# Kernel tuning notes

Measured on AMD Instinct MI355X. Metric: run time of the kernel, lower is better.

## Reference

```python
import jax, jax.numpy as jnp
import numpy as np


def setup_inputs() -> dict:
    key = jax.random.key(0)
    kq, kk, kv = jax.random.split(key, 3)
    N, T, F = 16, 2048, 128
    q = jax.random.normal(kq, (N, T, F), dtype=jnp.float32)
    k = jax.random.normal(kk, (N, T, F), dtype=jnp.float32)
    v = jax.random.normal(kv, (N, T, F), dtype=jnp.float32)
    return {"q": q, "k": k, "v": v, "masked": 1}


def reference(q, k, v, masked):
    # scores: [N, T, T] = q @ k^T / sqrt(F)
    F = q.shape[-1]
    scores = jnp.einsum("ntf,nsf->nts", q, k) / jnp.sqrt(jnp.asarray(F, q.dtype))
    if masked:
        T = q.shape[1]
        causal = jnp.tril(jnp.ones((T, T), dtype=bool))  # [T, T]
        scores = jnp.where(causal[None, :, :], scores, jnp.asarray(-1e9, scores.dtype))
    attn = jax.nn.softmax(scores, axis=-1)
    # dropout is identity in eval/reference mode
    return jnp.einsum("nts,nsf->ntf", attn, v)
```

## Files before the change

kernel.cpp:

```cpp
#include <hip/hip_runtime.h>
#include <hip/hip_bf16.h>
#include <stdint.h>

#define T_SEQ 2048
#define DH    128
#define BKV   64
#define QSCALE 0.12751742796f
#define SLOT_F 8320
#define WS_NEEDED 55115776ULL

typedef short  short8 __attribute__((ext_vector_type(8)));
typedef __bf16 bf16x8 __attribute__((ext_vector_type(8)));
typedef float  f32x4  __attribute__((ext_vector_type(4)));

__device__ __forceinline__ bf16x8 as_bf16x8(short8 x) { return __builtin_bit_cast(bf16x8, x); }

__device__ __forceinline__ uint32_t bf_bits(float x) {
  union { __hip_bfloat16 h; unsigned short u; } cv;
  cv.h = __float2bfloat16(x);
  return (uint32_t)cv.u;
}

__global__ void convert_bf16(const float* __restrict__ src, unsigned short* __restrict__ dst,
                             int n4) {
  int i = blockIdx.x * 256 + threadIdx.x;
  if (i >= n4) return;
  const float4 f = ((const float4*)src)[i];
  union { unsigned short us[4]; uint2 u2; } o;
  o.us[0] = (unsigned short)bf_bits(f.x);
  o.us[1] = (unsigned short)bf_bits(f.y);
  o.us[2] = (unsigned short)bf_bits(f.z);
  o.us[3] = (unsigned short)bf_bits(f.w);
  ((uint2*)dst)[i] = o.u2;
}

__global__ void transpose_v_bf16(const float* __restrict__ v, unsigned short* __restrict__ vt) {
  __shared__ float tile[64][65];
  const int n = blockIdx.z, d0 = blockIdx.y * 64, t0 = blockIdx.x * 64;
  const int tx = threadIdx.x, ty = threadIdx.y;
  #pragma unroll
  for (int i = 0; i < 64; i += 8)
    tile[ty + i][tx] = v[((size_t)n * T_SEQ + t0 + ty + i) * DH + d0 + tx];
  __syncthreads();
  #pragma unroll
  for (int i = 0; i < 64; i += 8)
    vt[((size_t)n * DH + d0 + ty + i) * T_SEQ + t0 + tx] = (unsigned short)bf_bits(tile[tx][ty + i]);
}

__global__ __launch_bounds__(256, 4) void attn_fwd(
    const float* __restrict__ Qf,
    const unsigned short* __restrict__ Kb,
    const unsigned short* __restrict__ Vt,
    float* __restrict__ Out,
    float* __restrict__ Part,
    const int* __restrict__ maskp,
    int use_split)
{
  __shared__ __align__(16) char smem[32768];

  const int tid  = threadIdx.x;
  const int lane = tid & 63;
  const int w    = tid >> 6;
  const int m15  = lane & 15;
  const int g    = lane >> 4;

  const int bid = blockIdx.x;
  const int n   = (bid & 7) + 8 * ((bid >> 3) & 1);
  const int job = bid >> 4;
  const int masked = maskp[0];

  int qt, c, k0, k1, nc;
  if (masked && use_split) {
    int base = 0; qt = 0;
    for (;;) { int ncq = (qt + 8) >> 3; if (job < base + ncq) { c = job - base; break; } base += ncq; ++qt; }
    nc = (qt + 8) >> 3;
    k0 = c * 8;
    k1 = min(k0 + 8, qt + 1);
  } else {
    if (job >= 32) return;
    qt = job; c = 0; nc = 1; k0 = 0;
    k1 = masked ? (qt + 1) : (T_SEQ / BKV);
  }

  const int qrow = qt * 64 + 16 * w + m15;

  bf16x8 qf[4];
  {
    const float* qg = Qf + ((size_t)n * T_SEQ + qrow) * DH;
    #pragma unroll
    for (int kf = 0; kf < 4; ++kf) {
      const float4 f0 = *(const float4*)(qg + 32 * kf + 8 * g);
      const float4 f1 = *(const float4*)(qg + 32 * kf + 8 * g + 4);
      union { unsigned short us[8]; short8 s8; } qa;
      qa.us[0] = (unsigned short)bf_bits(f0.x * QSCALE);
      qa.us[1] = (unsigned short)bf_bits(f0.y * QSCALE);
      qa.us[2] = (unsigned short)bf_bits(f0.z * QSCALE);
      qa.us[3] = (unsigned short)bf_bits(f0.w * QSCALE);
      qa.us[4] = (unsigned short)bf_bits(f1.x * QSCALE);
      qa.us[5] = (unsigned short)bf_bits(f1.y * QSCALE);
      qa.us[6] = (unsigned short)bf_bits(f1.z * QSCALE);
      qa.us[7] = (unsigned short)bf_bits(f1.w * QSCALE);
      qf[kf] = as_bf16x8(qa.s8);
    }
  }

  f32x4 acc[8] = {};
  float m_run = -3.0e38f;
  float ssum  = 0.f;
  const int swz = (m15 & 7) << 4;

  short8 kreg[4], vreg[4];
  const short8* gK = (const short8*)(Kb + (size_t)n * T_SEQ * DH);
  const short8* gV = (const short8*)(Vt + (size_t)n * DH * T_SEQ);

  auto loadRegs = [&](int kt) {
    const int t0 = kt * BKV;
    #pragma unroll
    for (int i = 0; i < 4; ++i) {
      int row = 16 * w + 4 * i + g;
      kreg[i] = gK[(size_t)(t0 + row) * 16 + m15];
    }
    #pragma unroll
    for (int i = 0; i < 4; ++i) {
      int d = 32 * w + 8 * i + (lane >> 3);
      vreg[i] = gV[(size_t)d * 256 + (t0 >> 3) + (lane & 7)];
    }
  };
  auto writeRegs = [&]() {
    #pragma unroll
    for (int i = 0; i < 4; ++i) {
      int row = 16 * w + 4 * i + g;
      int off = row * 256 + ((m15 * 16) ^ ((row & 7) << 4));
      *(short8*)(smem + off) = kreg[i];
    }
    #pragma unroll
    for (int i = 0; i < 4; ++i) {
      int d = 32 * w + 8 * i + (lane >> 3);
      int off = 16384 + d * 128 + (((lane & 7) * 16) ^ ((d & 7) << 4));
      *(short8*)(smem + off) = vreg[i];
    }
  };

  loadRegs(k0);
  writeRegs();

  for (int kt = k0; kt < k1; ++kt) {
    __syncthreads();
    if (kt + 1 < k1) loadRegs(kt + 1);

    const char* kb = smem;
    const char* vb = smem + 16384;

    f32x4 s[4] = {};
    #pragma unroll
    for (int kf = 0; kf < 4; ++kf) {
      #pragma unroll
      for (int ma = 0; ma < 4; ++ma) {
        short8 kfr = *(const short8*)(kb + (16 * ma + m15) * 256 + ((g * 16 + 64 * kf) ^ swz));
        s[ma] = __builtin_amdgcn_mfma_f32_16x16x32_bf16(as_bf16x8(kfr), qf[kf], s[ma], 0, 0, 0);
      }
    }

    if (masked && kt == qt) {
      #pragma unroll
      for (int ma = 0; ma < 4; ++ma)
        #pragma unroll
        for (int rr = 0; rr < 4; ++rr) {
          int kvg = kt * BKV + ma * 16 + g * 4 + rr;
          if (kvg > qrow) s[ma][rr] = -1.0e30f;
        }
    }

    float mx = s[0][0];
    #pragma unroll
    for (int ma = 0; ma < 4; ++ma)
      #pragma unroll
      for (int rr = 0; rr < 4; ++rr) mx = fmaxf(mx, s[ma][rr]);
    mx = fmaxf(mx, __shfl_xor(mx, 16));
    mx = fmaxf(mx, __shfl_xor(mx, 32));
    float mnew = fmaxf(m_run, mx);
    float corr = exp2f(m_run - mnew);

    float p[4][4];
    float lsum = 0.f;
    #pragma unroll
    for (int ma = 0; ma < 4; ++ma)
      #pragma unroll
      for (int rr = 0; rr < 4; ++rr) { p[ma][rr] = exp2f(s[ma][rr] - mnew); lsum += p[ma][rr]; }
    lsum += __shfl_xor(lsum, 16);
    lsum += __shfl_xor(lsum, 32);
    ssum = ssum * corr + lsum;
    m_run = mnew;
    #pragma unroll
    for (int i = 0; i < 8; ++i) {
      acc[i][0] *= corr; acc[i][1] *= corr; acc[i][2] *= corr; acc[i][3] *= corr;
    }

    uint32_t u[4][2];
    #pragma unroll
    for (int ma = 0; ma < 4; ++ma) {
      u[ma][0] = bf_bits(p[ma][0]) | (bf_bits(p[ma][1]) << 16);
      u[ma][1] = bf_bits(p[ma][2]) | (bf_bits(p[ma][3]) << 16);
    }

    const int srcA = ((g & 1) << 5) + m15;
    const int sel  = g >> 1;
    bf16x8 pfr[2];
    #pragma unroll
    for (int ks = 0; ks < 2; ++ks) {
      uint32_t a00 = (uint32_t)__shfl((int)u[2 * ks + 0][0], srcA);
      uint32_t a01 = (uint32_t)__shfl((int)u[2 * ks + 0][1], srcA);
      uint32_t a10 = (uint32_t)__shfl((int)u[2 * ks + 1][0], srcA);
      uint32_t a11 = (uint32_t)__shfl((int)u[2 * ks + 1][1], srcA);
      uint32_t b00 = (uint32_t)__shfl((int)u[2 * ks + 0][0], srcA + 16);
      uint32_t b01 = (uint32_t)__shfl((int)u[2 * ks + 0][1], srcA + 16);
      uint32_t b10 = (uint32_t)__shfl((int)u[2 * ks + 1][0], srcA + 16);
      uint32_t b11 = (uint32_t)__shfl((int)u[2 * ks + 1][1], srcA + 16);
      union { uint32_t q[4]; short8 s8; } pu;
      pu.q[0] = sel ? a10 : a00;
      pu.q[1] = sel ? a11 : a01;
      pu.q[2] = sel ? b10 : b00;
      pu.q[3] = sel ? b11 : b01;
      pfr[ks] = as_bf16x8(pu.s8);
    }

    #pragma unroll
    for (int dsub = 0; dsub < 8; ++dsub) {
      #pragma unroll
      for (int ks = 0; ks < 2; ++ks) {
        short8 vfr = *(const short8*)(vb + (16 * dsub + m15) * 128 + ((g * 16 + 64 * ks) ^ swz));
        acc[dsub] = __builtin_amdgcn_mfma_f32_16x16x32_bf16(as_bf16x8(vfr), pfr[ks], acc[dsub], 0, 0, 0);
      }
    }

    __syncthreads();
    if (kt + 1 < k1) writeRegs();
  }

  if (nc == 1) {
    const float inv = 1.0f / ssum;
    float* ob = Out + ((size_t)n * T_SEQ + qrow) * DH;
    #pragma unroll
    for (int dsub = 0; dsub < 8; ++dsub) {
      f32x4 o;
      o[0] = acc[dsub][0] * inv; o[1] = acc[dsub][1] * inv;
      o[2] = acc[dsub][2] * inv; o[3] = acc[dsub][3] * inv;
      *(f32x4*)(ob + dsub * 16 + g * 4) = o;
    }
  } else {
    int b8 = 0;
    for (int q = 8; q < qt; ++q) b8 += (q + 8) >> 3;
    float* slot = Part + ((size_t)n * 72 + b8 + c) * SLOT_F;
    if (g == 0) { slot[16 * w + m15] = m_run; slot[64 + 16 * w + m15] = ssum; }
    float* so = slot + 128 + (size_t)(16 * w + m15) * 128;
    #pragma unroll
    for (int dsub = 0; dsub < 8; ++dsub)
      *(f32x4*)(so + dsub * 16 + 4 * g) = acc[dsub];
  }
}

__global__ void combine_kernel(const float* __restrict__ Part, float* __restrict__ Out,
                               const int* __restrict__ maskp, int use_split) {
  if (!maskp[0] || !use_split) return;
  const int cb = blockIdx.x;
  const int n  = cb & 15;
  const int qt = (cb >> 4) + 8;
  const int nc = (qt + 8) >> 3;
  int b8 = 0;
  for (int q = 8; q < qt; ++q) b8 += (q + 8) >> 3;
  const float* slot0 = Part + ((size_t)n * 72 + b8) * SLOT_F;

  const int tid = threadIdx.x;
  const int q   = tid >> 2;
  const int d0  = (tid & 3) * 32;

  float m[4], s[4], wgt[4];
  float M = -3.0e38f;
  for (int i = 0; i < nc; ++i) {
    m[i] = slot0[(size_t)i * SLOT_F + q];
    s[i] = slot0[(size_t)i * SLOT_F + 64 + q];
    M = fmaxf(M, m[i]);
  }
  float denom = 0.f;
  for (int i = 0; i < nc; ++i) { wgt[i] = exp2f(m[i] - M); denom += s[i] * wgt[i]; }
  const float inv = 1.0f / denom;

  float* ob = Out + ((size_t)n * T_SEQ + qt * 64 + q) * DH + d0;
  #pragma unroll
  for (int j = 0; j < 8; ++j) {
    f32x4 a = {};
    for (int i = 0; i < nc; ++i) {
      const f32x4 v = *(const f32x4*)(slot0 + (size_t)i * SLOT_F + 128 + (size_t)q * 128 + d0 + 4 * j);
      a[0] += v[0] * wgt[i]; a[1] += v[1] * wgt[i]; a[2] += v[2] * wgt[i]; a[3] += v[3] * wgt[i];
    }
    a[0] *= inv; a[1] *= inv; a[2] *= inv; a[3] *= inv;
    *(f32x4*)(ob + 4 * j) = a;
  }
}

extern "C" void kernel_launch(void* const* d_in, const int* in_sizes, int n_in,
                              void* d_out, int out_size, void* d_ws, size_t ws_size,
                              hipStream_t stream) {
  (void)in_sizes; (void)n_in; (void)out_size;
  const float* q = (const float*)d_in[0];
  const float* k = (const float*)d_in[1];
  const float* v = (const float*)d_in[2];
  const int* maskp = (const int*)d_in[3];
  float* out = (float*)d_out;

  const size_t elems = (size_t)16 * T_SEQ * DH;
  unsigned short* Kb = (unsigned short*)d_ws;
  unsigned short* Vt = Kb + elems;
  float* Part = (float*)d_ws + elems;
  const int use_split = (ws_size >= WS_NEEDED) ? 1 : 0;

  const int n4 = (int)(elems / 4);
  convert_bf16<<<n4 / 256, 256, 0, stream>>>(k, Kb, n4);
  transpose_v_bf16<<<dim3(T_SEQ / 64, DH / 64, 16), dim3(64, 8), 0, stream>>>(v, Vt);
  attn_fwd<<<dim3(1280), 256, 0, stream>>>(q, Kb, Vt, out, Part, maskp, use_split);
  combine_kernel<<<dim3(384), 256, 0, stream>>>(Part, out, maskp, use_split);
}
```

Measured before the change: 186.8 us.

## Use 128-row query tiles with 8 waves, fuse K/V prep, add MFMA priority

Doubles the query tile to 128 rows per block using 512 threads (8 waves), so each K/V tile staged in shared memory is reused by twice as many query rows. The split-KV work table, partial-slot layout and combine kernel are reworked to match. The K convert and V transpose kernels are merged into one launch, and s_setprio is raised around the MFMA sections. In exchange, the causal mask check now runs on two diagonal tiles, there are fewer blocks to balance the load, and register pressure rises under launch bounds of 512 threads with 6 waves.

Result: slower. 234.9 us (+25.7%).

```diff
diff --git a/kernel.cpp b/kernel.cpp
--- a/kernel.cpp
+++ b/kernel.cpp
@@ -6,7 +6,7 @@
 #define DH    128
 #define BKV   64
 #define QSCALE 0.12751742796f
-#define SLOT_F 8320
+#define SLOT_F 16640
 #define WS_NEEDED 55115776ULL
 
 typedef short  short8 __attribute__((ext_vector_type(8)));
@@ -21,33 +21,34 @@
   return (uint32_t)cv.u;
 }
 
-__global__ void convert_bf16(const float* __restrict__ src, unsigned short* __restrict__ dst,
-                             int n4) {
-  int i = blockIdx.x * 256 + threadIdx.x;
-  if (i >= n4) return;
-  const float4 f = ((const float4*)src)[i];
-  union { unsigned short us[4]; uint2 u2; } o;
-  o.us[0] = (unsigned short)bf_bits(f.x);
-  o.us[1] = (unsigned short)bf_bits(f.y);
-  o.us[2] = (unsigned short)bf_bits(f.z);
-  o.us[3] = (unsigned short)bf_bits(f.w);
-  ((uint2*)dst)[i] = o.u2;
-}
-
-__global__ void transpose_v_bf16(const float* __restrict__ v, unsigned short* __restrict__ vt) {
+__global__ void prep_kv(const float* __restrict__ k, const float* __restrict__ v,
+                        unsigned short* __restrict__ kb, unsigned short* __restrict__ vt) {
   __shared__ float tile[64][65];
-  const int n = blockIdx.z, d0 = blockIdx.y * 64, t0 = blockIdx.x * 64;
-  const int tx = threadIdx.x, ty = threadIdx.y;
-  #pragma unroll
-  for (int i = 0; i < 64; i += 8)
-    tile[ty + i][tx] = v[((size_t)n * T_SEQ + t0 + ty + i) * DH + d0 + tx];
-  __syncthreads();
-  #pragma unroll
-  for (int i = 0; i < 64; i += 8)
-    vt[((size_t)n * DH + d0 + ty + i) * T_SEQ + t0 + tx] = (unsigned short)bf_bits(tile[tx][ty + i]);
-}
-
-__global__ __launch_bounds__(256, 4) void attn_fwd(
+  const int n = blockIdx.y, x = blockIdx.x, tid = threadIdx.x;
+  if (x < 256) {
+    const int i = (n * 256 + x) * 256 + tid;
+    const float4 f = ((const float4*)k)[i];
+    union { unsigned short us[4]; uint2 u2; } o;
+    o.us[0] = (unsigned short)bf_bits(f.x);
+    o.us[1] = (unsigned short)bf_bits(f.y);
+    o.us[2] = (unsigned short)bf_bits(f.z);
+    o.us[3] = (unsigned short)bf_bits(f.w);
+    ((uint2*)kb)[i] = o.u2;
+  } else {
+    const int x2 = x - 256;
+    const int t0 = (x2 & 31) * 64, d0 = (x2 >> 5) * 64;
+    const int tx = tid & 63, ty = tid >> 6;
+    #pragma unroll
+    for (int i = 0; i < 64; i += 4)
+      tile[ty + i][tx] = v[((size_t)n * T_SEQ + t0 + ty + i) * DH + d0 + tx];
+    __syncthreads();
+    #pragma unroll
+    for (int i = 0; i < 64; i += 4)
+      vt[((size_t)n * DH + d0 + ty + i) * T_SEQ + t0 + tx] = (unsigned short)bf_bits(tile[tx][ty + i]);
+  }
+}
+
+__global__ __launch_bounds__(512, 6) void attn_fwd(
     const float* __restrict__ Qf,
     const unsigned short* __restrict__ Kb,
     const unsigned short* __restrict__ Vt,
@@ -69,20 +70,20 @@
   const int job = bid >> 4;
   const int masked = maskp[0];
 
-  int qt, c, k0, k1, nc;
+  int Q, c, k0, k1, nc;
   if (masked && use_split) {
-    int base = 0; qt = 0;
-    for (;;) { int ncq = (qt + 8) >> 3; if (job < base + ncq) { c = job - base; break; } base += ncq; ++qt; }
-    nc = (qt + 8) >> 3;
+    int base = 0; Q = 0;
+    for (;;) { int ncq = (2 * Q + 9) >> 3; if (job < base + ncq) { c = job - base; break; } base += ncq; ++Q; }
+    nc = (2 * Q + 9) >> 3;
     k0 = c * 8;
-    k1 = min(k0 + 8, qt + 1);
+    k1 = min(k0 + 8, 2 * Q + 2);
   } else {
-    if (job >= 32) return;
-    qt = job; c = 0; nc = 1; k0 = 0;
-    k1 = masked ? (qt + 1) : (T_SEQ / BKV);
-  }
-
-  const int qrow = qt * 64 + 16 * w + m15;
+    if (job >= 16) return;
+    Q = job; c = 0; nc = 1; k0 = 0;
+    k1 = masked ? (2 * Q + 2) : (T_SEQ / BKV);
+  }
+
+  const int qrow = Q * 128 + 16 * w + m15;
 
   bf16x8 qf[4];
   {
@@ -109,33 +110,33 @@
   float ssum  = 0.f;
   const int swz = (m15 & 7) << 4;
 
-  short8 kreg[4], vreg[4];
+  short8 kreg[2], vreg[2];
   const short8* gK = (const short8*)(Kb + (size_t)n * T_SEQ * DH);
   const short8* gV = (const short8*)(Vt + (size_t)n * DH * T_SEQ);
 
   auto loadRegs = [&](int kt) {
     const int t0 = kt * BKV;
     #pragma unroll
-    for (int i = 0; i < 4; ++i) {
-      int row = 16 * w + 4 * i + g;
+    for (int i = 0; i < 2; ++i) {
+      int row = 8 * w + 4 * i + g;
       kreg[i] = gK[(size_t)(t0 + row) * 16 + m15];
     }
     #pragma unroll
-    for (int i = 0; i < 4; ++i) {
-      int d = 32 * w + 8 * i + (lane >> 3);
+    for (int i = 0; i < 2; ++i) {
+      int d = 16 * w + 8 * i + (lane >> 3);
       vreg[i] = gV[(size_t)d * 256 + (t0 >> 3) + (lane & 7)];
     }
   };
   auto writeRegs = [&]() {
     #pragma unroll
-    for (int i = 0; i < 4; ++i) {
-      int row = 16 * w + 4 * i + g;
+    for (int i = 0; i < 2; ++i) {
+      int row = 8 * w + 4 * i + g;
       int off = row * 256 + ((m15 * 16) ^ ((row & 7) << 4));
       *(short8*)(smem + off) = kreg[i];
     }
     #pragma unroll
-    for (int i = 0; i < 4; ++i) {
-      int d = 32 * w + 8 * i + (lane >> 3);
+    for (int i = 0; i < 2; ++i) {
+      int d = 16 * w + 8 * i + (lane >> 3);
       int off = 16384 + d * 128 + (((lane & 7) * 16) ^ ((d & 7) << 4));
       *(short8*)(smem + off) = vreg[i];
     }
@@ -152,6 +153,7 @@
     const char* vb = smem + 16384;
 
     f32x4 s[4] = {};
+    __builtin_amdgcn_s_setprio(1);
     #pragma unroll
     for (int kf = 0; kf < 4; ++kf) {
       #pragma unroll
@@ -160,8 +162,9 @@
         s[ma] = __builtin_amdgcn_mfma_f32_16x16x32_bf16(as_bf16x8(kfr), qf[kf], s[ma], 0, 0, 0);
       }
     }
-
-    if (masked && kt == qt) {
+    __builtin_amdgcn_s_setprio(0);
+
+    if (masked && kt >= 2 * Q) {
       #pragma unroll
       for (int ma = 0; ma < 4; ++ma)
         #pragma unroll
@@ -224,6 +227,7 @@
       pfr[ks] = as_bf16x8(pu.s8);
     }
 
+    __builtin_amdgcn_s_setprio(1);
     #pragma unroll
     for (int dsub = 0; dsub < 8; ++dsub) {
       #pragma unroll
@@ -232,6 +236,7 @@
         acc[dsub] = __builtin_amdgcn_mfma_f32_16x16x32_bf16(as_bf16x8(vfr), pfr[ks], acc[dsub], 0, 0, 0);
       }
     }
+    __builtin_amdgcn_s_setprio(0);
 
     __syncthreads();
     if (kt + 1 < k1) writeRegs();
@@ -249,10 +254,11 @@
     }
   } else {
     int b8 = 0;
-    for (int q = 8; q < qt; ++q) b8 += (q + 8) >> 3;
-    float* slot = Part + ((size_t)n * 72 + b8 + c) * SLOT_F;
-    if (g == 0) { slot[16 * w + m15] = m_run; slot[64 + 16 * w + m15] = ssum; }
-    float* so = slot + 128 + (size_t)(16 * w + m15) * 128;
+    for (int qq = 4; qq < Q; ++qq) b8 += (2 * qq + 9) >> 3;
+    float* slot = Part + ((size_t)n * 36 + b8 + c) * SLOT_F;
+    const int qr = 16 * w + m15;
+    if (g == 0) { slot[qr] = m_run; slot[128 + qr] = ssum; }
+    float* so = slot + 256 + (size_t)qr * 128;
     #pragma unroll
     for (int dsub = 0; dsub < 8; ++dsub)
       *(f32x4*)(so + dsub * 16 + 4 * g) = acc[dsub];
@@ -264,33 +270,33 @@
   if (!maskp[0] || !use_split) return;
   const int cb = blockIdx.x;
   const int n  = cb & 15;
-  const int qt = (cb >> 4) + 8;
-  const int nc = (qt + 8) >> 3;
+  const int Q  = (cb >> 4) + 4;
+  const int nc = (2 * Q + 9) >> 3;
   int b8 = 0;
-  for (int q = 8; q < qt; ++q) b8 += (q + 8) >> 3;
-  const float* slot0 = Part + ((size_t)n * 72 + b8) * SLOT_F;
+  for (int qq = 4; qq < Q; ++qq) b8 += (2 * qq + 9) >> 3;
+  const float* slot0 = Part + ((size_t)n * 36 + b8) * SLOT_F;
 
   const int tid = threadIdx.x;
-  const int q   = tid >> 2;
-  const int d0  = (tid & 3) * 32;
+  const int q   = tid >> 1;
+  const int d0  = (tid & 1) * 64;
 
   float m[4], s[4], wgt[4];
   float M = -3.0e38f;
   for (int i = 0; i < nc; ++i) {
     m[i] = slot0[(size_t)i * SLOT_F + q];
-    s[i] = slot0[(size_t)i * SLOT_F + 64 + q];
+    s[i] = slot0[(size_t)i * SLOT_F + 128 + q];
     M = fmaxf(M, m[i]);
   }
   float denom = 0.f;
   for (int i = 0; i < nc; ++i) { wgt[i] = exp2f(m[i] - M); denom += s[i] * wgt[i]; }
   const float inv = 1.0f / denom;
 
-  float* ob = Out + ((size_t)n * T_SEQ + qt * 64 + q) * DH + d0;
+  float* ob = Out + ((size_t)n * T_SEQ + Q * 128 + q) * DH + d0;
   #pragma unroll
-  for (int j = 0; j < 8; ++j) {
+  for (int j = 0; j < 16; ++j) {
     f32x4 a = {};
     for (int i = 0; i < nc; ++i) {
-      const f32x4 v = *(const f32x4*)(slot0 + (size_t)i * SLOT_F + 128 + (size_t)q * 128 + d0 + 4 * j);
+      const f32x4 v = *(const f32x4*)(slot0 + (size_t)i * SLOT_F + 256 + (size_t)q * 128 + d0 + 4 * j);
       a[0] += v[0] * wgt[i]; a[1] += v[1] * wgt[i]; a[2] += v[2] * wgt[i]; a[3] += v[3] * wgt[i];
     }
     a[0] *= inv; a[1] *= inv; a[2] *= inv; a[3] *= inv;
@@ -314,9 +320,7 @@
   float* Part = (float*)d_ws + elems;
   const int use_split = (ws_size >= WS_NEEDED) ? 1 : 0;
 
-  const int n4 = (int)(elems / 4);
-  convert_bf16<<<n4 / 256, 256, 0, stream>>>(k, Kb, n4);
-  transpose_v_bf16<<<dim3(T_SEQ / 64, DH / 64, 16), dim3(64, 8), 0, stream>>>(v, Vt);
-  attn_fwd<<<dim3(1280), 256, 0, stream>>>(q, Kb, Vt, out, Part, maskp, use_split);
-  combine_kernel<<<dim3(384), 256, 0, stream>>>(Part, out, maskp, use_split);
-}
+  prep_kv<<<dim3(320, 16), 256, 0, stream>>>(k, v, Kb, Vt);
+  attn_fwd<<<dim3(640), 512, 0, stream>>>(q, Kb, Vt, out, Part, maskp, use_split);
+  combine_kernel<<<dim3(192), 256, 0, stream>>>(Part, out, maskp, use_split);
+}
```
